# Kernel tuning notes

Measured on AMD Instinct MI355X. Metric: run time of the kernel, lower is better.

Reference implementation:

```python
import jax, jax.numpy as jnp
import numpy as np

NUM_SEGMENTS = 16
N_MAX = 256
CHUNK = (N_MAX + NUM_SEGMENTS - 1) // NUM_SEGMENTS  # 16
BETA1, BETA2, BETA3 = 0.5, 0.5, 0.4


def _masked_mean(x, mask):
    m = mask.astype(x.dtype)
    s = m.sum()
    return jnp.where(s > 0, (x * m).sum() / jnp.maximum(s, 1.0), jnp.zeros((), x.dtype))


def setup_inputs() -> dict:
    key = jax.random.key(0)
    ks = jax.random.split(key, 10)
    B, S, H, V, Sm, R = 2, 1024, 4096, 32000, 256, 256
    k_hidden = jax.random.normal(ks[0], (B, S, H), dtype=jnp.float32)
    last_hidden = jax.random.normal(ks[1], (B, S, H), dtype=jnp.float32)
    input_ids = jax.random.randint(ks[2], (B, S), 0, V)
    attention_mask = jnp.ones((B, S), dtype=jnp.int32)
    starts = jax.random.randint(ks[3], (B,), 0, 300)
    ends = starts + 200 + jax.random.randint(ks[4], (B,), 0, 100)
    math_lengths = jnp.full((B,), Sm, dtype=jnp.int64 if jax.config.jax_enable_x64 else jnp.int32)
    math_labels = jax.random.randint(ks[5], (B, Sm), 0, V)
    math_attention_mask = jnp.ones((B, Sm), dtype=jnp.int32)
    A_matrices = jax.random.normal(ks[6], (NUM_SEGMENTS, H, R), dtype=jnp.float32) * 0.02
    B_matrices = jax.random.normal(ks[7], (NUM_SEGMENTS, R, H), dtype=jnp.float32) * 0.02
    bias = jnp.zeros((NUM_SEGMENTS, H), dtype=jnp.float32)
    W_lm = jax.random.normal(ks[8], (H, V), dtype=jnp.float32) * 0.02
    return {"k_hidden": k_hidden, "last_hidden": last_hidden, "input_ids": input_ids,
            "attention_mask": attention_mask, "starts": starts, "ends": ends,
            "math_lengths": math_lengths, "math_labels": math_labels,
            "math_attention_mask": math_attention_mask, "A_matrices": A_matrices,
            "B_matrices": B_matrices, "bias": bias, "W_lm": W_lm}


def reference(k_hidden, last_hidden, input_ids, attention_mask, starts, ends,
              math_lengths, math_labels, math_attention_mask,
              A_matrices, B_matrices, bias, W_lm):
    B, S, H = last_hidden.shape
    Sm = math_labels.shape[1]
    n_blk = Sm // CHUNK  # == NUM_SEGMENTS here (N_max == Sm)

    # ---- simple-talk / final-answer CE losses on full logits ----
    logits = jnp.einsum('bsh,hv->bsv', last_hidden, W_lm)  # [B,S,V]
    logp = jax.nn.log_softmax(logits[:, :-1, :], axis=-1)
    labels = input_ids[:, 1:]
    nll = -jnp.take_along_axis(logp, labels[..., None], axis=-1)[..., 0]  # [B,S-1]
    idx = jnp.arange(S - 1)[None, :]
    real_len = attention_mask.sum(axis=1)[:, None]
    mask_simple = (idx >= starts[:, None] - 1) & (idx <= ends[:, None] - 1)
    mask_final = (idx >= ends[:, None]) & (idx < real_len - 1)
    simple_talk_loss = _masked_mean(nll, mask_simple)
    final_answer_loss = _masked_mean(nll, mask_final)

    # ---- math loss: segment-routed LoRA (A @ (B @ h) + bias) then lm_head CE ----
    # mask_hidden selects the contiguous block [starts, starts+math_lengths) per row;
    # with full math_attention_mask this is exactly Sm tokens per row.
    pos = starts[:, None] + jnp.arange(Sm)[None, :]  # [B,Sm]
    math_h = jnp.take_along_axis(k_hidden, pos[:, :, None], axis=1)  # [B,Sm,H]
    # segment_ids are position//CHUNK -> contiguous blocks: grouped GEMM via reshape
    hb = math_h.reshape(B, n_blk, CHUNK, H)
    inter = jnp.einsum('bsch,srh->bscr', hb, B_matrices)      # B_seg @ h
    trans = jnp.einsum('bscr,shr->bsch', inter, A_matrices)   # A_seg @ inter
    trans = trans + bias[None, :, None, :]
    t = trans.reshape(B * Sm, H)
    mlogits = t @ W_lm                                        # [B*Sm, V]
    mlogp = jax.nn.log_softmax(mlogits, axis=-1)
    tgt = math_labels.reshape(-1)
    mnll = -jnp.take_along_axis(mlogp, tgt[:, None], axis=-1)[:, 0]  # [B*Sm]
    math_loss = mnll.mean()
    # per-segment mean losses (diagnostic, no-grad in original)
    A_losses = jax.lax.stop_gradient(mnll.reshape(B, n_blk, CHUNK).mean(axis=(0, 2)))

    total_loss = BETA1 * math_loss + BETA2 * simple_talk_loss + BETA3 * final_answer_loss
    return total_loss, math_loss, simple_talk_loss, final_answer_loss, A_losses
```

## Files before the change

### kernel.cpp

```cpp
#include <hip/hip_runtime.h>

#define NSEG 16
#define CH   16
#define Bb   2
#define Ss   1024
#define Hh   4096
#define Vv   32000
#define SMm  256
#define Rr   256

#define M_MAIN 2046
#define M_MATH 512
#define M_REAL 2558
#define M_PAD  2560

#define BM 256
#define BN 128
#define BK 128
#define NT_M (M_PAD/BM)
#define NT_N (Vv/BN)
#define KT   (Hh/BK)
#define NWG  (NT_M*NT_N)
#define NQG  (Hh/16)

#define HC   8
#define HCL  (Hh/HC)
#define PART_STRIDE (Bb*NSEG*CH*Rr)

typedef __attribute__((ext_vector_type(4))) float    floatx4;
typedef __attribute__((ext_vector_type(4))) int      intx4;
typedef __attribute__((ext_vector_type(8))) int      intx8;

#define ASCALE 16.f
#define WSCALE 256.f
#define DESCALE (1.f/(16.f*256.f))

template<bool W>
__device__ __forceinline__ int cvtpk(float a, float b, int old) {
  return __builtin_amdgcn_cvt_pk_fp8_f32(a, b, old, W);
}

__device__ __forceinline__ void gload_lds16(const void* g, void* l) {
  __builtin_amdgcn_global_load_lds((const __attribute__((address_space(1))) void*)g,
                                   (__attribute__((address_space(3))) void*)l, 16, 0, 0);
}

__global__ __launch_bounds__(256) void k_convA(const float* __restrict__ lh, intx4* __restrict__ Aq) {
  int row = blockIdx.x * 256 + threadIdx.x;
  int qgg = blockIdx.y;
  if (row >= M_MAIN) return;
  int b = row / (Ss - 1), s = row % (Ss - 1);
  const floatx4* src = (const floatx4*)(lh + ((size_t)(b * Ss + s)) * Hh + qgg * 16);
  floatx4 f0 = src[0], f1 = src[1], f2 = src[2], f3 = src[3];
  int p0 = cvtpk<false>(f0[0]*ASCALE, f0[1]*ASCALE, 0); p0 = cvtpk<true>(f0[2]*ASCALE, f0[3]*ASCALE, p0);
  int p1 = cvtpk<false>(f1[0]*ASCALE, f1[1]*ASCALE, 0); p1 = cvtpk<true>(f1[2]*ASCALE, f1[3]*ASCALE, p1);
  int p2 = cvtpk<false>(f2[0]*ASCALE, f2[1]*ASCALE, 0); p2 = cvtpk<true>(f2[2]*ASCALE, f2[3]*ASCALE, p2);
  int p3 = cvtpk<false>(f3[0]*ASCALE, f3[1]*ASCALE, 0); p3 = cvtpk<true>(f3[2]*ASCALE, f3[3]*ASCALE, p3);
  Aq[(size_t)qgg * M_PAD + row] = (intx4){p0, p1, p2, p3};
}

__global__ __launch_bounds__(256) void k_convW(const float* __restrict__ W, intx4* __restrict__ Wf) {
  int v = blockIdx.x * 256 + threadIdx.x;
  int qgg = blockIdx.y;
  const float* base = W + (size_t)(qgg * 16) * Vv + v;
  int p[4];
  #pragma unroll
  for (int q = 0; q < 4; ++q) {
    float e0 = base[(size_t)(4*q+0) * Vv] * WSCALE;
    float e1 = base[(size_t)(4*q+1) * Vv] * WSCALE;
    float e2 = base[(size_t)(4*q+2) * Vv] * WSCALE;
    float e3 = base[(size_t)(4*q+3) * Vv] * WSCALE;
    int pp = cvtpk<false>(e0, e1, 0);
    p[q] = cvtpk<true>(e2, e3, pp);
  }
  Wf[(size_t)qgg * Vv + v] = (intx4){p[0], p[1], p[2], p[3]};
}

__global__ __launch_bounds__(256) void k_inter2(const float* __restrict__ kh, const float* __restrict__ Bm,
                                                const int* __restrict__ starts, float* __restrict__ part) {
  int bid = blockIdx.x;
  int b = bid >> 7, seg = (bid >> 3) & 15, hc = bid & 7;
  int tid = threadIdx.x;
  __shared__ float sX[CH][HCL];
  int st = starts[b];
  for (int i = tid; i < CH * (HCL / 4); i += 256) {
    int c = i / (HCL / 4), k4 = i % (HCL / 4);
    int pos = st + seg * CH + c;
    ((floatx4*)&sX[c][0])[k4] = *(const floatx4*)(kh + ((size_t)(b * Ss + pos)) * Hh + hc * HCL + 4 * k4);
  }
  __syncthreads();
  const floatx4* w = (const floatx4*)(Bm + ((size_t)(seg * Rr + tid)) * Hh + hc * HCL);
  float acc[CH];
  #pragma unroll
  for (int c = 0; c < CH; ++c) acc[c] = 0.f;
  for (int i = 0; i < HCL / 4; ++i) {
    floatx4 w4 = w[i];
    #pragma unroll
    for (int c = 0; c < CH; ++c)
      acc[c] += w4[0]*sX[c][4*i] + w4[1]*sX[c][4*i+1] + w4[2]*sX[c][4*i+2] + w4[3]*sX[c][4*i+3];
  }
  float* dst = part + (size_t)hc * PART_STRIDE + ((size_t)(b * NSEG + seg)) * CH * Rr;
  #pragma unroll
  for (int c = 0; c < CH; ++c) dst[c * Rr + tid] = acc[c];
}

__global__ __launch_bounds__(256) void k_trans(const float* __restrict__ part, const float* __restrict__ Am,
                                               const float* __restrict__ bias, intx4* __restrict__ Aq) {
  int bid = blockIdx.x;
  int b = bid >> 7, seg = (bid >> 3) & 15, ht = bid & 7;
  int tid = threadIdx.x;
  __shared__ float sI[CH][Rr];
  const float* ib = part + ((size_t)(b * NSEG + seg)) * CH * Rr;
  for (int i = tid; i < CH * Rr / 4; i += 256) {
    floatx4 s = ((const floatx4*)ib)[i];
    #pragma unroll
    for (int hc = 1; hc < HC; ++hc)
      s += ((const floatx4*)(ib + (size_t)hc * PART_STRIDE))[i];
    ((floatx4*)&sI[0][0])[i] = s;
  }
  __syncthreads();
  unsigned char* Ab = (unsigned char*)Aq;
  for (int hh = 0; hh < 2; ++hh) {
    int h = (ht << 9) + (tid << 1) + hh;
    const floatx4* ar = (const floatx4*)(Am + ((size_t)(seg * Hh + h)) * Rr);
    float acc[CH];
    #pragma unroll
    for (int c = 0; c < CH; ++c) acc[c] = 0.f;
    for (int i = 0; i < Rr / 4; ++i) {
      floatx4 a4 = ar[i];
      #pragma unroll
      for (int c = 0; c < CH; ++c)
        acc[c] += a4[0]*sI[c][i*4] + a4[1]*sI[c][i*4+1] + a4[2]*sI[c][i*4+2] + a4[3]*sI[c][i*4+3];
    }
    float bv = bias[seg * Hh + h];
    #pragma unroll
    for (int c = 0; c < CH; ++c) {
      int row = M_MAIN + b * SMm + seg * CH + c;
      int pk = cvtpk<false>((acc[c] + bv) * ASCALE, 0.f, 0);
      Ab[(((size_t)(h >> 4)) * M_PAD + row) * 16 + (h & 15)] = (unsigned char)(pk & 0xFF);
    }
  }
}

__global__ __launch_bounds__(256) void k_labels(const int* __restrict__ input_ids, const int* __restrict__ mlab,
                                                int* __restrict__ labels, float* __restrict__ llog,
                                                intx4* __restrict__ Aq) {
  int t = blockIdx.x * 256 + threadIdx.x;
  if (t < M_PAD) {
    int lab;
    if (t < M_MAIN)      { int b = t / (Ss - 1), s = t % (Ss - 1); lab = input_ids[b * Ss + s + 1]; }
    else if (t < M_REAL) { lab = mlab[t - M_MAIN]; }
    else                 { lab = 0x7fffffff; }
    labels[t] = lab;
    llog[t] = 0.f;
  }
  if (t < 2 * NQG) {
    int qgg = t >> 1, row = M_REAL + (t & 1);
    Aq[(size_t)qgg * M_PAD + row] = (intx4){0, 0, 0, 0};
  }
}

__global__ __launch_bounds__(512, 2) void k_gemm_mx2(const intx4* __restrict__ Aq, const intx4* __restrict__ Wf,
                                                     const int* __restrict__ labels, float* __restrict__ pmax,
                                                     float* __restrict__ psum, float* __restrict__ llog) {
  __shared__ intx4 As[3][8][BM];
  __shared__ intx4 Bs[3][8][BN];
  __shared__ float redM[BM * 2];
  __shared__ float redS[BM * 2];

  int bid = blockIdx.x;
  int xcd = bid & 7, loc = bid >> 3;
  int swz = (xcd < 4) ? (xcd * 313 + loc) : (1252 + (xcd - 4) * 312 + loc);
  int mt = swz % NT_M, nt = swz / NT_M;
  int m0 = mt * BM, n0 = nt * BN;
  int tid = threadIdx.x;
  int lane = tid & 63;
  int wid = tid >> 6;
  int wr = wid >> 1, wc = wid & 1;
  int l15 = lane & 15, l4 = lane >> 4;

  floatx4 acc[4][4];
  #pragma unroll
  for (int m = 0; m < 4; ++m)
    #pragma unroll
    for (int n = 0; n < 4; ++n) acc[m][n] = (floatx4){0.f, 0.f, 0.f, 0.f};

#define STAGE(tt, bb) do {                                                              \
    const intx4* ab_ = Aq + (size_t)(tt) * 8 * M_PAD;                                   \
    _Pragma("unroll")                                                                   \
    for (int it_ = 0; it_ < 4; ++it_) {                                                 \
      int s_ = it_ * 512 + tid;                                                         \
      gload_lds16(ab_ + ((size_t)(s_ >> 8) * M_PAD + m0 + (s_ & 255)),                  \
                  (void*)(&As[bb][0][0] + s_));                                         \
    }                                                                                   \
    const intx4* wb_ = Wf + (size_t)(tt) * 8 * Vv;                                      \
    _Pragma("unroll")                                                                   \
    for (int it_ = 0; it_ < 2; ++it_) {                                                 \
      int s_ = it_ * 512 + tid;                                                         \
      gload_lds16(wb_ + ((size_t)(s_ >> 7) * Vv + n0 + (s_ & 127)),                     \
                  (void*)(&Bs[bb][0][0] + s_));                                         \
    }                                                                                   \
  } while (0)

  STAGE(0, 0);
  STAGE(1, 1);
  int cur = 0;

  for (int kt = 0; kt < KT; ++kt) {
    if (kt < KT - 1) {
      asm volatile("s_waitcnt vmcnt(6)" ::: "memory");
    } else {
      asm volatile("s_waitcnt vmcnt(0)" ::: "memory");
    }
    __builtin_amdgcn_s_barrier();
    __builtin_amdgcn_sched_barrier(0);

    intx8 a[4], b[4];
    #pragma unroll
    for (int m = 0; m < 4; ++m) {
      int row = wr * 64 + m * 16 + l15;
      intx4 lo = As[cur][2 * l4][row];
      intx4 hi = As[cur][2 * l4 + 1][row];
      a[m] = __builtin_shufflevector(lo, hi, 0, 1, 2, 3, 4, 5, 6, 7);
    }
    #pragma unroll
    for (int n = 0; n < 4; ++n) {
      int col = wc * 64 + n * 16 + l15;
      intx4 lo = Bs[cur][2 * l4][col];
      intx4 hi = Bs[cur][2 * l4 + 1][col];
      b[n] = __builtin_shufflevector(lo, hi, 0, 1, 2, 3, 4, 5, 6, 7);
    }

    if (kt + 2 < KT) STAGE(kt + 2, (cur + 2) % 3);

    __builtin_amdgcn_s_setprio(1);
    #pragma unroll
    for (int m = 0; m < 4; ++m)
      #pragma unroll
      for (int n = 0; n < 4; ++n)
        acc[m][n] = __builtin_amdgcn_mfma_scale_f32_16x16x128_f8f6f4(
            a[m], b[n], acc[m][n], 0, 0, 0, 0x7F7F7F7F, 0, 0x7F7F7F7F);
    __builtin_amdgcn_s_setprio(0);

    cur = (cur + 1) % 3;
  }
#undef STAGE

  #pragma unroll
  for (int m = 0; m < 4; ++m)
    #pragma unroll
    for (int n = 0; n < 4; ++n) acc[m][n] *= DESCALE;

  __syncthreads();

  #pragma unroll
  for (int m = 0; m < 4; ++m) {
    #pragma unroll
    for (int r = 0; r < 4; ++r) {
      int grow = m0 + wr * 64 + m * 16 + l4 * 4 + r;
      int lab = (grow < M_REAL) ? labels[grow] : -1;
      #pragma unroll
      for (int n = 0; n < 4; ++n) {
        int gcol = n0 + wc * 64 + n * 16 + l15;
        if (lab == gcol) llog[grow] = acc[m][n][r];
      }
    }
  }
  float rm[4][4];
  #pragma unroll
  for (int m = 0; m < 4; ++m)
    #pragma unroll
    for (int r = 0; r < 4; ++r) {
      float v = fmaxf(fmaxf(acc[m][0][r], acc[m][1][r]), fmaxf(acc[m][2][r], acc[m][3][r]));
      v = fmaxf(v, __shfl_xor(v, 1));
      v = fmaxf(v, __shfl_xor(v, 2));
      v = fmaxf(v, __shfl_xor(v, 4));
      v = fmaxf(v, __shfl_xor(v, 8));
      rm[m][r] = v;
    }
  if (l15 == 0) {
    #pragma unroll
    for (int m = 0; m < 4; ++m)
      #pragma unroll
      for (int r = 0; r < 4; ++r)
        redM[(wr * 64 + m * 16 + l4 * 4 + r) * 2 + wc] = rm[m][r];
  }
  __syncthreads();
  #pragma unroll
  for (int m = 0; m < 4; ++m)
    #pragma unroll
    for (int r = 0; r < 4; ++r) {
      int row = wr * 64 + m * 16 + l4 * 4 + r;
      float tmx = fmaxf(redM[row * 2], redM[row * 2 + 1]);
      float s = 0.f;
      #pragma unroll
      for (int n = 0; n < 4; ++n) s += __expf(acc[m][n][r] - tmx);
      s += __shfl_xor(s, 1);
      s += __shfl_xor(s, 2);
      s += __shfl_xor(s, 4);
      s += __shfl_xor(s, 8);
      rm[m][r] = s;
    }
  if (l15 == 0) {
    #pragma unroll
    for (int m = 0; m < 4; ++m)
      #pragma unroll
      for (int r = 0; r < 4; ++r)
        redS[(wr * 64 + m * 16 + l4 * 4 + r) * 2 + wc] = rm[m][r];
  }
  __syncthreads();
  if (tid < BM) {
    int grow = m0 + tid;
    if (grow < M_REAL) {
      float tmx = fmaxf(redM[tid * 2], redM[tid * 2 + 1]);
      float s = redS[tid * 2] + redS[tid * 2 + 1];
      pmax[(size_t)grow * NT_N + nt] = tmx;
      psum[(size_t)grow * NT_N + nt] = s;
    }
  }
}

__global__ __launch_bounds__(256) void k_fin(const float* __restrict__ pmax, const float* __restrict__ psum,
                                             const float* __restrict__ llog, float* __restrict__ nll) {
  int row = blockIdx.x * 4 + (threadIdx.x >> 6);
  int lane = threadIdx.x & 63;
  if (row >= M_REAL) return;
  float m = -3.4e38f;
  for (int t = lane; t < NT_N; t += 64) m = fmaxf(m, pmax[(size_t)row * NT_N + t]);
  #pragma unroll
  for (int d = 1; d < 64; d <<= 1) m = fmaxf(m, __shfl_xor(m, d));
  float s = 0.f;
  for (int t = lane; t < NT_N; t += 64)
    s += psum[(size_t)row * NT_N + t] * __expf(pmax[(size_t)row * NT_N + t] - m);
  #pragma unroll
  for (int d = 1; d < 64; d <<= 1) s += __shfl_xor(s, d);
  if (lane == 0) nll[row] = logf(s) + m - llog[row];
}

__global__ __launch_bounds__(256) void k_loss(const float* __restrict__ nll, const int* __restrict__ starts,
                                              const int* __restrict__ ends, const int* __restrict__ attn,
                                              float* __restrict__ out) {
  __shared__ float rA[256], rB[256], rC[256], rD[256];
  __shared__ float smath[M_MATH];
  __shared__ float rl[2];
  int tid = threadIdx.x;
  for (int b = 0; b < 2; ++b) {
    float p = 0.f;
    for (int i = tid; i < Ss; i += 256) p += (float)attn[b * Ss + i];
    rA[tid] = p;
    __syncthreads();
    if (tid == 0) { float t = 0.f; for (int i = 0; i < 256; ++i) t += rA[i]; rl[b] = t; }
    __syncthreads();
  }
  float ss = 0.f, sc = 0.f, fs = 0.f, fc = 0.f;
  int st0 = starts[0], st1 = starts[1], en0 = ends[0], en1 = ends[1];
  for (int r = tid; r < M_MAIN; r += 256) {
    int b = r / (Ss - 1), idx = r % (Ss - 1);
    int st = b ? st1 : st0, en = b ? en1 : en0;
    int rlen = (int)rl[b];
    float v = nll[r];
    if (idx >= st - 1 && idx <= en - 1) { ss += v; sc += 1.f; }
    if (idx >= en && idx < rlen - 1)    { fs += v; fc += 1.f; }
  }
  rA[tid] = ss; rB[tid] = sc; rC[tid] = fs; rD[tid] = fc;
  for (int j = tid; j < M_MATH; j += 256) smath[j] = nll[M_MAIN + j];
  __syncthreads();
  if (tid == 0) {
    float SS = 0.f, SC = 0.f, FS = 0.f, FC = 0.f;
    for (int i = 0; i < 256; ++i) { SS += rA[i]; SC += rB[i]; FS += rC[i]; FC += rD[i]; }
    float MS = 0.f;
    for (int j = 0; j < M_MATH; ++j) MS += smath[j];
    float math_loss = MS / (float)M_MATH;
    float simple = (SC > 0.f) ? SS / fmaxf(SC, 1.f) : 0.f;
    float fin    = (FC > 0.f) ? FS / fmaxf(FC, 1.f) : 0.f;
    out[0] = 0.5f * math_loss + 0.5f * simple + 0.4f * fin;
    out[1] = math_loss;
    out[2] = simple;
    out[3] = fin;
    for (int seg = 0; seg < NSEG; ++seg) {
      float a = 0.f;
      for (int b = 0; b < 2; ++b)
        for (int c = 0; c < CH; ++c) a += smath[b * SMm + seg * CH + c];
      out[4 + seg] = a / 32.f;
    }
  }
}

extern "C" void kernel_launch(void* const* d_in, const int* in_sizes, int n_in,
                              void* d_out, int out_size, void* d_ws, size_t ws_size,
                              hipStream_t stream) {
  const float* k_hidden    = (const float*)d_in[0];
  const float* last_hidden = (const float*)d_in[1];
  const int*   input_ids   = (const int*)d_in[2];
  const int*   attn        = (const int*)d_in[3];
  const int*   starts      = (const int*)d_in[4];
  const int*   ends        = (const int*)d_in[5];
  const int*   math_labels = (const int*)d_in[7];
  const float* A_matrices  = (const float*)d_in[9];
  const float* B_matrices  = (const float*)d_in[10];
  const float* bias        = (const float*)d_in[11];
  const float* W_lm        = (const float*)d_in[12];
  float* out = (float*)d_out;

  char* ws = (char*)d_ws;
  size_t off = 0;
  intx4* Wf   = (intx4*)ws;                 off += (size_t)NQG * Vv * 16;
  intx4* Aq   = (intx4*)(ws + off);         off += (size_t)NQG * M_PAD * 16;
  float* part = (float*)(ws + off);         off += (size_t)HC * PART_STRIDE * 4;
  int*   labels = (int*)(ws + off);         off += (size_t)M_PAD * 4;
  float* llog   = (float*)(ws + off);       off += (size_t)M_PAD * 4;
  float* pmax   = (float*)(ws + off);       off += (size_t)M_PAD * NT_N * 4;
  float* psum   = (float*)(ws + off);       off += (size_t)M_PAD * NT_N * 4;
  float* nll    = (float*)(ws + off);       off += (size_t)M_PAD * 4;

  {
    dim3 ga((M_MAIN + 255) / 256, NQG);
    k_convA<<<ga, 256, 0, stream>>>(last_hidden, Aq);
  }
  k_inter2<<<Bb * NSEG * HC, 256, 0, stream>>>(k_hidden, B_matrices, starts, part);
  k_trans<<<Bb * NSEG * 8, 256, 0, stream>>>(part, A_matrices, bias, Aq);
  k_labels<<<(M_PAD + 255) / 256, 256, 0, stream>>>(input_ids, math_labels, labels, llog, Aq);
  {
    dim3 gw(Vv / 256, NQG);
    k_convW<<<gw, 256, 0, stream>>>(W_lm, Wf);
  }
  k_gemm_mx2<<<NWG, 512, 0, stream>>>(Aq, Wf, labels, pmax, psum, llog);
  k_fin<<<(M_REAL + 3) / 4, 256, 0, stream>>>(pmax, psum, llog, nll);
  k_loss<<<1, 256, 0, stream>>>(nll, starts, ends, attn, out);
}
```

Before: 590.5 us.

## Enlarge MX-FP8 GEMM tile to 256x256 with double buffering and phased A loads

```diff
diff --git a/kernel.cpp b/kernel.cpp
--- a/kernel.cpp
+++ b/kernel.cpp
@@ -15,7 +15,7 @@
 #define M_PAD  2560
 
 #define BM 256
-#define BN 128
+#define BN 256
 #define BK 128
 #define NT_M (M_PAD/BM)
 #define NT_N (Vv/BN)
@@ -160,104 +160,108 @@
   }
 }
 
-__global__ __launch_bounds__(512, 2) void k_gemm_mx2(const intx4* __restrict__ Aq, const intx4* __restrict__ Wf,
-                                                     const int* __restrict__ labels, float* __restrict__ pmax,
-                                                     float* __restrict__ psum, float* __restrict__ llog) {
-  __shared__ intx4 As[3][8][BM];
-  __shared__ intx4 Bs[3][8][BN];
-  __shared__ float redM[BM * 2];
-  __shared__ float redS[BM * 2];
+__global__ __launch_bounds__(512, 2) void k_gemm_8p(const intx4* __restrict__ Aq, const intx4* __restrict__ Wf,
+                                                    const int* __restrict__ labels, float* __restrict__ pmax,
+                                                    float* __restrict__ psum, float* __restrict__ llog) {
+  __shared__ intx4 As[2][8][BM];
+  __shared__ intx4 Bs[2][8][BN];
 
   int bid = blockIdx.x;
   int xcd = bid & 7, loc = bid >> 3;
-  int swz = (xcd < 4) ? (xcd * 313 + loc) : (1252 + (xcd - 4) * 312 + loc);
+  int swz = (xcd < 2) ? (xcd * 157 + loc) : (314 + (xcd - 2) * 156 + loc);
   int mt = swz % NT_M, nt = swz / NT_M;
   int m0 = mt * BM, n0 = nt * BN;
   int tid = threadIdx.x;
   int lane = tid & 63;
   int wid = tid >> 6;
-  int wr = wid >> 1, wc = wid & 1;
+  int wr = wid >> 2, wc = wid & 3;
   int l15 = lane & 15, l4 = lane >> 4;
 
-  floatx4 acc[4][4];
-  #pragma unroll
-  for (int m = 0; m < 4; ++m)
+  floatx4 acc[8][4];
+  #pragma unroll
+  for (int m = 0; m < 8; ++m)
     #pragma unroll
     for (int n = 0; n < 4; ++n) acc[m][n] = (floatx4){0.f, 0.f, 0.f, 0.f};
 
-#define STAGE(tt, bb) do {                                                              \
+#define STAGE(bb, tt) do {                                                              \
     const intx4* ab_ = Aq + (size_t)(tt) * 8 * M_PAD;                                   \
+    const intx4* wb_ = Wf + (size_t)(tt) * 8 * Vv;                                      \
     _Pragma("unroll")                                                                   \
     for (int it_ = 0; it_ < 4; ++it_) {                                                 \
-      int s_ = it_ * 512 + tid;                                                         \
-      gload_lds16(ab_ + ((size_t)(s_ >> 8) * M_PAD + m0 + (s_ & 255)),                  \
-                  (void*)(&As[bb][0][0] + s_));                                         \
+      int ci_ = it_ * 512 + tid;                                                        \
+      gload_lds16(ab_ + (size_t)(ci_ >> 8) * M_PAD + m0 + (ci_ & 255),                  \
+                  (void*)(&As[bb][0][0] + ci_));                                        \
     }                                                                                   \
-    const intx4* wb_ = Wf + (size_t)(tt) * 8 * Vv;                                      \
     _Pragma("unroll")                                                                   \
-    for (int it_ = 0; it_ < 2; ++it_) {                                                 \
-      int s_ = it_ * 512 + tid;                                                         \
-      gload_lds16(wb_ + ((size_t)(s_ >> 7) * Vv + n0 + (s_ & 127)),                     \
-                  (void*)(&Bs[bb][0][0] + s_));                                         \
+    for (int it_ = 0; it_ < 4; ++it_) {                                                 \
+      int ci_ = it_ * 512 + tid;                                                        \
+      gload_lds16(wb_ + (size_t)(ci_ >> 8) * Vv + n0 + (ci_ & 255),                     \
+                  (void*)(&Bs[bb][0][0] + ci_));                                        \
     }                                                                                   \
   } while (0)
 
   STAGE(0, 0);
   STAGE(1, 1);
-  int cur = 0;
 
   for (int kt = 0; kt < KT; ++kt) {
+    int cb = kt & 1;
     if (kt < KT - 1) {
-      asm volatile("s_waitcnt vmcnt(6)" ::: "memory");
+      asm volatile("s_waitcnt vmcnt(8)" ::: "memory");
     } else {
       asm volatile("s_waitcnt vmcnt(0)" ::: "memory");
     }
     __builtin_amdgcn_s_barrier();
     __builtin_amdgcn_sched_barrier(0);
 
-    intx8 a[4], b[4];
-    #pragma unroll
-    for (int m = 0; m < 4; ++m) {
-      int row = wr * 64 + m * 16 + l15;
-      intx4 lo = As[cur][2 * l4][row];
-      intx4 hi = As[cur][2 * l4 + 1][row];
-      a[m] = __builtin_shufflevector(lo, hi, 0, 1, 2, 3, 4, 5, 6, 7);
-    }
+    intx8 bf[4];
     #pragma unroll
     for (int n = 0; n < 4; ++n) {
       int col = wc * 64 + n * 16 + l15;
-      intx4 lo = Bs[cur][2 * l4][col];
-      intx4 hi = Bs[cur][2 * l4 + 1][col];
-      b[n] = __builtin_shufflevector(lo, hi, 0, 1, 2, 3, 4, 5, 6, 7);
-    }
-
-    if (kt + 2 < KT) STAGE(kt + 2, (cur + 2) % 3);
-
-    __builtin_amdgcn_s_setprio(1);
-    #pragma unroll
-    for (int m = 0; m < 4; ++m)
+      intx4 lo = Bs[cb][2 * l4][col];
+      intx4 hi = Bs[cb][2 * l4 + 1][col];
+      bf[n] = __builtin_shufflevector(lo, hi, 0, 1, 2, 3, 4, 5, 6, 7);
+    }
+
+    #pragma unroll
+    for (int ph = 0; ph < 4; ++ph) {
+      int r0 = wr * 128 + (2 * ph) * 16 + l15;
+      int r1 = r0 + 16;
+      intx4 lo0 = As[cb][2 * l4][r0], hi0 = As[cb][2 * l4 + 1][r0];
+      intx4 lo1 = As[cb][2 * l4][r1], hi1 = As[cb][2 * l4 + 1][r1];
+      intx8 a0 = __builtin_shufflevector(lo0, hi0, 0, 1, 2, 3, 4, 5, 6, 7);
+      intx8 a1 = __builtin_shufflevector(lo1, hi1, 0, 1, 2, 3, 4, 5, 6, 7);
+      __builtin_amdgcn_s_setprio(1);
       #pragma unroll
       for (int n = 0; n < 4; ++n)
-        acc[m][n] = __builtin_amdgcn_mfma_scale_f32_16x16x128_f8f6f4(
-            a[m], b[n], acc[m][n], 0, 0, 0, 0x7F7F7F7F, 0, 0x7F7F7F7F);
-    __builtin_amdgcn_s_setprio(0);
-
-    cur = (cur + 1) % 3;
+        acc[2 * ph][n] = __builtin_amdgcn_mfma_scale_f32_16x16x128_f8f6f4(
+            a0, bf[n], acc[2 * ph][n], 0, 0, 0, 0x7F7F7F7F, 0, 0x7F7F7F7F);
+      #pragma unroll
+      for (int n = 0; n < 4; ++n)
+        acc[2 * ph + 1][n] = __builtin_amdgcn_mfma_scale_f32_16x16x128_f8f6f4(
+            a1, bf[n], acc[2 * ph + 1][n], 0, 0, 0, 0x7F7F7F7F, 0, 0x7F7F7F7F);
+      __builtin_amdgcn_s_setprio(0);
+    }
+
+    __builtin_amdgcn_s_barrier();
+    __builtin_amdgcn_sched_barrier(0);
+    if (kt + 2 < KT) STAGE(cb, kt + 2);
   }
 #undef STAGE
 
   #pragma unroll
-  for (int m = 0; m < 4; ++m)
+  for (int m = 0; m < 8; ++m)
     #pragma unroll
     for (int n = 0; n < 4; ++n) acc[m][n] *= DESCALE;
 
   __syncthreads();
-
-  #pragma unroll
-  for (int m = 0; m < 4; ++m) {
+  float* redM = (float*)&As[0][0][0];
+  float* redS = redM + BM * 4;
+
+  #pragma unroll
+  for (int m = 0; m < 8; ++m) {
     #pragma unroll
     for (int r = 0; r < 4; ++r) {
-      int grow = m0 + wr * 64 + m * 16 + l4 * 4 + r;
+      int grow = m0 + wr * 128 + m * 16 + l4 * 4 + r;
       int lab = (grow < M_REAL) ? labels[grow] : -1;
       #pragma unroll
       for (int n = 0; n < 4; ++n) {
@@ -266,9 +270,9 @@
       }
     }
   }
-  float rm[4][4];
-  #pragma unroll
-  for (int m = 0; m < 4; ++m)
+  float rm[8][4];
+  #pragma unroll
+  for (int m = 0; m < 8; ++m)
     #pragma unroll
     for (int r = 0; r < 4; ++r) {
       float v = fmaxf(fmaxf(acc[m][0][r], acc[m][1][r]), fmaxf(acc[m][2][r], acc[m][3][r]));
@@ -280,18 +284,19 @@
     }
   if (l15 == 0) {
     #pragma unroll
-    for (int m = 0; m < 4; ++m)
+    for (int m = 0; m < 8; ++m)
       #pragma unroll
       for (int r = 0; r < 4; ++r)
-        redM[(wr * 64 + m * 16 + l4 * 4 + r) * 2 + wc] = rm[m][r];
-  }
-  __syncthreads();
-  #pragma unroll
-  for (int m = 0; m < 4; ++m)
+        redM[(wr * 128 + m * 16 + l4 * 4 + r) * 4 + wc] = rm[m][r];
+  }
+  __syncthreads();
+  #pragma unroll
+  for (int m = 0; m < 8; ++m)
     #pragma unroll
     for (int r = 0; r < 4; ++r) {
-      int row = wr * 64 + m * 16 + l4 * 4 + r;
-      float tmx = fmaxf(redM[row * 2], redM[row * 2 + 1]);
+      int row = wr * 128 + m * 16 + l4 * 4 + r;
+      float tmx = fmaxf(fmaxf(redM[row * 4], redM[row * 4 + 1]),
+                        fmaxf(redM[row * 4 + 2], redM[row * 4 + 3]));
       float s = 0.f;
       #pragma unroll
       for (int n = 0; n < 4; ++n) s += __expf(acc[m][n][r] - tmx);
@@ -303,17 +308,18 @@
     }
   if (l15 == 0) {
     #pragma unroll
-    for (int m = 0; m < 4; ++m)
+    for (int m = 0; m < 8; ++m)
       #pragma unroll
       for (int r = 0; r < 4; ++r)
-        redS[(wr * 64 + m * 16 + l4 * 4 + r) * 2 + wc] = rm[m][r];
+        redS[(wr * 128 + m * 16 + l4 * 4 + r) * 4 + wc] = rm[m][r];
   }
   __syncthreads();
   if (tid < BM) {
     int grow = m0 + tid;
     if (grow < M_REAL) {
-      float tmx = fmaxf(redM[tid * 2], redM[tid * 2 + 1]);
-      float s = redS[tid * 2] + redS[tid * 2 + 1];
+      float tmx = fmaxf(fmaxf(redM[tid * 4], redM[tid * 4 + 1]),
+                        fmaxf(redM[tid * 4 + 2], redM[tid * 4 + 3]));
+      float s = redS[tid * 4] + redS[tid * 4 + 1] + redS[tid * 4 + 2] + redS[tid * 4 + 3];
       pmax[(size_t)grow * NT_N + nt] = tmx;
       psum[(size_t)grow * NT_N + nt] = s;
     }
@@ -424,7 +430,7 @@
     dim3 gw(Vv / 256, NQG);
     k_convW<<<gw, 256, 0, stream>>>(W_lm, Wf);
   }
-  k_gemm_mx2<<<NWG, 512, 0, stream>>>(Aq, Wf, labels, pmax, psum, llog);
+  k_gemm_8p<<<NWG, 512, 0, stream>>>(Aq, Wf, labels, pmax, psum, llog);
   k_fin<<<(M_REAL + 3) / 4, 256, 0, stream>>>(pmax, psum, llog, nll);
   k_loss<<<1, 256, 0, stream>>>(nll, starts, ends, attn, out);
 }
```

After: 761.0 us. 28.9% more time.
